# Kernel optimization log

Measured on AMD Instinct MI355X. Metric: run time of the kernel, lower is better.

## Reference

```python
import jax, jax.numpy as jnp
import numpy as np

THRESHOLD = 0.01
TOPK_RATIO = 0.7

def setup_inputs() -> dict:
    key = jax.random.key(0)
    k1, k2, k3, k4, k5 = jax.random.split(key, 5)
    B, N, F, K = 8, 2048, 512, 256
    x = jax.random.normal(k1, (B, N, F), dtype=jnp.float32)
    adj = jax.random.uniform(k2, (B, N, N), dtype=jnp.float32)
    mask = jnp.ones((B, N), dtype=jnp.float32)
    # assign_main = Linear(F->K), ReLU, Linear(K->K)
    W1 = jax.random.normal(k3, (F, K), dtype=jnp.float32) / np.sqrt(F)
    b1 = jnp.zeros((K,), dtype=jnp.float32)
    W2 = jax.random.normal(k4, (K, K), dtype=jnp.float32) / np.sqrt(K)
    b2 = jnp.zeros((K,), dtype=jnp.float32)
    return {"x": x, "adj": adj, "mask": mask, "W1": W1, "b1": b1, "W2": W2, "b2": b2}

def reference(x, adj, mask, W1, b1, W2, b2):
    B, N, Fdim = x.shape
    K = W2.shape[1]
    # soft assignment logits with masked softmax over clusters
    h = jax.nn.relu(jnp.einsum('bnf,fk->bnk', x, W1) + b1)
    logits = jnp.einsum('bnk,kl->bnl', h, W2) + b2            # [B,N,K]
    logits = logits + (-1e9) * (1.0 - mask[..., None])
    S = jax.nn.softmax(logits, axis=-1)                       # [B,N,K]
    # pooled features and pooled adjacency
    pfeat = jnp.einsum('bnk,bnf->bkf', S, x)                  # S^T x -> [B,K,F]
    mid = jnp.einsum('bnm,bmk->bnk', adj, S)                  # adj @ S
    pooled = jnp.einsum('bnk,bnl->bkl', S, mid)               # S^T adj S -> [B,K,K]
    # threshold + top-k sparsify with straight-through estimator
    topk = min(K, int(np.ceil(TOPK_RATIO * K)))
    thr_mask = (pooled >= THRESHOLD).astype(pooled.dtype)
    a_thr = pooled * thr_mask
    _, idx = jax.lax.top_k(a_thr, topk)                       # [B,K,topk]
    bi = jnp.arange(B)[:, None, None]
    ri = jnp.arange(K)[None, :, None]
    fmask = jnp.zeros_like(pooled).at[bi, ri, idx].set(1.0)
    a_sp = pooled * fmask
    a_ste = a_sp + jax.lax.stop_gradient(pooled - a_sp)       # forward == pooled
    # symmetric degree renormalization
    row_sum = a_ste.sum(axis=-1)
    d_inv_sqrt = 1.0 / jnp.sqrt(row_sum + 1e-9)
    pooled_adj = a_ste * d_inv_sqrt[:, :, None] * d_inv_sqrt[:, None, :]
    pmask = jnp.ones((B, K), dtype=x.dtype)
    return pfeat, pooled_adj, pmask
```

## Files before the change

kernel.cpp:

```cpp
#include <hip/hip_runtime.h>
#include <hip/hip_bf16.h>


typedef float f32x4 __attribute__((ext_vector_type(4)));
typedef __bf16 bf16x8 __attribute__((ext_vector_type(8)));

__device__ __forceinline__ void async_load16(const void* g, void* l) {
  __builtin_amdgcn_global_load_lds((const __attribute__((address_space(1))) void*)g,
                                   (__attribute__((address_space(3))) void*)l, 16, 0, 0);
}
__device__ __forceinline__ unsigned short f2bf(float f) {
  return __builtin_bit_cast(unsigned short, (__bf16)f);
}
__device__ __forceinline__ ushort4 f4_to_bf4(float4 v) {
  ushort4 u; u.x = f2bf(v.x); u.y = f2bf(v.y); u.z = f2bf(v.z); u.w = f2bf(v.w); return u;
}

template <int ROWS, int BK, int NT>
__device__ __forceinline__ void stage_bf16(const __bf16* __restrict__ src, long long ld,
                                           __bf16* lds, int t) {
  constexpr int GR = BK / 8;
  constexpr int N = ROWS * GR / NT;
#pragma unroll
  for (int c = 0; c < N; ++c) {
    const int idx = c * NT + t;
    const int row = idx / GR;
    const int g = idx % GR;
    const int gs = g ^ (row & (GR - 1) & 7);
    async_load16(src + (long long)row * ld + gs * 8, lds + idx * 8);
  }
}
template <int BK>
__device__ __forceinline__ bf16x8 frag(const __bf16* lds, int row, int kq) {
  constexpr int GR = BK / 8;
  const int g = kq ^ (row & (GR - 1) & 7);
  return *(const bf16x8*)(lds + row * BK + g * 8);
}

__global__ __launch_bounds__(256) void prep_weights_k(const float* __restrict__ W1,
                                                      const float* __restrict__ W2,
                                                      __bf16* __restrict__ W1T,
                                                      __bf16* __restrict__ W2T) {
  __shared__ float tile[64][65];
  int bid = blockIdx.x;
  const float* in; __bf16* out; int R, C;
  if (bid < 32) { in = W1; out = W1T; R = 512; C = 256; }
  else { bid -= 32; in = W2; out = W2T; R = 256; C = 256; }
  const int r0 = (bid >> 2) * 64, c0 = (bid & 3) * 64;
  const int tr = threadIdx.x >> 6, tc = threadIdx.x & 63;
#pragma unroll
  for (int i = 0; i < 16; ++i)
    tile[tr + i * 4][tc] = in[(long long)(r0 + tr + i * 4) * C + c0 + tc];
  __syncthreads();
#pragma unroll
  for (int i = 0; i < 16; ++i)
    out[(long long)(c0 + tr + i * 4) * R + r0 + tc] = (__bf16)tile[tc][tr + i * 4];
}

__global__ __launch_bounds__(256) void assign_fused_k(
    const float* __restrict__ x, const __bf16* __restrict__ W1T,
    const __bf16* __restrict__ W2T, const float* __restrict__ b1,
    const float* __restrict__ b2, const float* __restrict__ mask,
    __bf16* __restrict__ ST) {
  __shared__ alignas(16) __bf16 Ax[2][32 * 32];
  __shared__ alignas(16) __bf16 Bw[2][256 * 32];
  __shared__ alignas(16) __bf16 hl[32 * 264];
  __shared__ float red[2][4][32];

  const int t = threadIdx.x;
  const int lane = t & 63, wave = t >> 6;
  const int l15 = lane & 15, l4 = lane >> 4;
  const int wn = wave * 64;
  const long long row0 = (long long)blockIdx.y * 32;
  const float* Xb = x + row0 * 512;

  const int arow = t >> 3, afq = t & 7;
  const int aoff = arow * 32 + (((afq >> 1) ^ (arow & 3)) * 8) + (afq & 1) * 4;

  f32x4 acc[2][4] = {};

  float4 va = *(const float4*)(Xb + (long long)arow * 512 + afq * 4);
  stage_bf16<256, 32, 256>(W1T, 512, Bw[0], t);
  *(ushort4*)&Ax[0][aoff] = f4_to_bf4(va);
  __syncthreads();

  for (int tt = 0; tt < 16; ++tt) {
    const int cur = tt & 1, nxt = cur ^ 1;
    float4 na;
    if (tt < 15) {
      const int kk = (tt + 1) * 32;
      na = *(const float4*)(Xb + (long long)arow * 512 + kk + afq * 4);
      stage_bf16<256, 32, 256>(W1T + kk, 512, Bw[nxt], t);
    }
    bf16x8 af[2], bfr[4];
#pragma unroll
    for (int i = 0; i < 2; ++i) af[i] = frag<32>(Ax[cur], i * 16 + l15, l4);
#pragma unroll
    for (int j = 0; j < 4; ++j) bfr[j] = frag<32>(Bw[cur], wn + j * 16 + l15, l4);
#pragma unroll
    for (int i = 0; i < 2; ++i)
#pragma unroll
      for (int j = 0; j < 4; ++j)
        acc[i][j] = __builtin_amdgcn_mfma_f32_16x16x32_bf16(af[i], bfr[j], acc[i][j], 0, 0, 0);
    if (tt < 15) *(ushort4*)&Ax[nxt][aoff] = f4_to_bf4(na);
    __syncthreads();
  }

  stage_bf16<256, 32, 256>(W2T, 256, Bw[0], t);
#pragma unroll
  for (int j = 0; j < 4; ++j) {
    const int col = wn + j * 16 + l15;
    const float bv = b1[col];
#pragma unroll
    for (int i = 0; i < 2; ++i)
#pragma unroll
      for (int r = 0; r < 4; ++r)
        hl[(i * 16 + l4 * 4 + r) * 264 + col] = (__bf16)fmaxf(acc[i][j][r] + bv, 0.f);
  }
  __syncthreads();

  f32x4 acc2[2][4] = {};
  for (int tt = 0; tt < 8; ++tt) {
    const int cur = tt & 1, nxt = cur ^ 1;
    if (tt < 7) stage_bf16<256, 32, 256>(W2T + (tt + 1) * 32, 256, Bw[nxt], t);
    bf16x8 af[2], bfr[4];
#pragma unroll
    for (int i = 0; i < 2; ++i)
      af[i] = *(const bf16x8*)(&hl[(i * 16 + l15) * 264 + tt * 32 + l4 * 8]);
#pragma unroll
    for (int j = 0; j < 4; ++j) bfr[j] = frag<32>(Bw[cur], wn + j * 16 + l15, l4);
#pragma unroll
    for (int i = 0; i < 2; ++i)
#pragma unroll
      for (int j = 0; j < 4; ++j)
        acc2[i][j] = __builtin_amdgcn_mfma_f32_16x16x32_bf16(af[i], bfr[j], acc2[i][j], 0, 0, 0);
    __syncthreads();
  }

  float mb[2][4], mx[2][4], sm[2][4];
#pragma unroll
  for (int i = 0; i < 2; ++i)
#pragma unroll
    for (int r = 0; r < 4; ++r) {
      mb[i][r] = -1e9f * (1.0f - mask[row0 + i * 16 + l4 * 4 + r]);
      mx[i][r] = -3.4e38f;
      sm[i][r] = 0.f;
    }
#pragma unroll
  for (int j = 0; j < 4; ++j) {
    const float bv = b2[wn + j * 16 + l15];
#pragma unroll
    for (int i = 0; i < 2; ++i)
#pragma unroll
      for (int r = 0; r < 4; ++r) {
        const float v = acc2[i][j][r] + bv + mb[i][r];
        acc2[i][j][r] = v;
        mx[i][r] = fmaxf(mx[i][r], v);
      }
  }
#pragma unroll
  for (int i = 0; i < 2; ++i)
#pragma unroll
    for (int r = 0; r < 4; ++r) {
      float m = mx[i][r];
      m = fmaxf(m, __shfl_xor(m, 1, 64)); m = fmaxf(m, __shfl_xor(m, 2, 64));
      m = fmaxf(m, __shfl_xor(m, 4, 64)); m = fmaxf(m, __shfl_xor(m, 8, 64));
      mx[i][r] = m;
    }
  if (l15 == 0)
#pragma unroll
    for (int i = 0; i < 2; ++i)
#pragma unroll
      for (int r = 0; r < 4; ++r) red[0][wave][i * 16 + l4 * 4 + r] = mx[i][r];
  __syncthreads();
#pragma unroll
  for (int i = 0; i < 2; ++i)
#pragma unroll
    for (int r = 0; r < 4; ++r) {
      const int rl = i * 16 + l4 * 4 + r;
      mx[i][r] = fmaxf(fmaxf(red[0][0][rl], red[0][1][rl]),
                       fmaxf(red[0][2][rl], red[0][3][rl]));
    }
#pragma unroll
  for (int j = 0; j < 4; ++j)
#pragma unroll
    for (int i = 0; i < 2; ++i)
#pragma unroll
      for (int r = 0; r < 4; ++r) {
        const float e = __expf(acc2[i][j][r] - mx[i][r]);
        acc2[i][j][r] = e;
        sm[i][r] += e;
      }
#pragma unroll
  for (int i = 0; i < 2; ++i)
#pragma unroll
    for (int r = 0; r < 4; ++r) {
      float s = sm[i][r];
      s += __shfl_xor(s, 1, 64); s += __shfl_xor(s, 2, 64);
      s += __shfl_xor(s, 4, 64); s += __shfl_xor(s, 8, 64);
      sm[i][r] = s;
    }
  if (l15 == 0)
#pragma unroll
    for (int i = 0; i < 2; ++i)
#pragma unroll
      for (int r = 0; r < 4; ++r) red[1][wave][i * 16 + l4 * 4 + r] = sm[i][r];
  __syncthreads();
  float inv[2][4];
#pragma unroll
  for (int i = 0; i < 2; ++i)
#pragma unroll
    for (int r = 0; r < 4; ++r) {
      const int rl = i * 16 + l4 * 4 + r;
      inv[i][r] = 1.0f / (red[1][0][rl] + red[1][1][rl] + red[1][2][rl] + red[1][3][rl]);
    }
  const long long bb = row0 >> 11;
  const long long n0 = row0 & 2047;
  __bf16* Sb = ST + bb * 524288;
#pragma unroll
  for (int j = 0; j < 4; ++j) {
    const int col = wn + j * 16 + l15;
#pragma unroll
    for (int i = 0; i < 2; ++i) {
      ushort4 u;
      u.x = f2bf(acc2[i][j][0] * inv[i][0]);
      u.y = f2bf(acc2[i][j][1] * inv[i][1]);
      u.z = f2bf(acc2[i][j][2] * inv[i][2]);
      u.w = f2bf(acc2[i][j][3] * inv[i][3]);
      *(ushort4*)(Sb + (long long)col * 2048 + n0 + i * 16 + l4 * 4) = u;
    }
  }
}

__global__ __launch_bounds__(256) void gemm_adj_k(const float* __restrict__ adj,
                                                  const __bf16* __restrict__ ST,
                                                  __bf16* __restrict__ midT) {
  __shared__ alignas(16) __bf16 Aa[2][32 * 64];
  __shared__ alignas(16) __bf16 Bs[2][256 * 64];
  const int t = threadIdx.x;
  const int lane = t & 63, wave = t >> 6;
  const int l15 = lane & 15, l4 = lane >> 4;
  const int wn = wave * 64;
  const int bz = blockIdx.z;
  const long long r0 = (long long)blockIdx.y * 32;
  const float* Ab = adj + (long long)bz * 4194304 + r0 * 2048;
  const __bf16* Bb = ST + (long long)bz * 524288;

  const int arow = t >> 4, afq = t & 15;
  const int arow1 = arow + 16;
  const int aoff0 = arow * 64 + (((afq >> 1) ^ (arow & 7)) * 8) + (afq & 1) * 4;
  const int aoff1 = arow1 * 64 + (((afq >> 1) ^ (arow1 & 7)) * 8) + (afq & 1) * 4;

  f32x4 acc[2][4] = {};

  float4 va0 = *(const float4*)(Ab + (long long)arow * 2048 + afq * 4);
  float4 va1 = *(const float4*)(Ab + (long long)arow1 * 2048 + afq * 4);
  stage_bf16<256, 64, 256>(Bb, 2048, Bs[0], t);
  *(ushort4*)&Aa[0][aoff0] = f4_to_bf4(va0);
  *(ushort4*)&Aa[0][aoff1] = f4_to_bf4(va1);
  __syncthreads();

  for (int tt = 0; tt < 32; ++tt) {
    const int cur = tt & 1, nxt = cur ^ 1;
    float4 na0, na1;
    if (tt < 31) {
      const int kk = (tt + 1) * 64;
      na0 = *(const float4*)(Ab + (long long)arow * 2048 + kk + afq * 4);
      na1 = *(const float4*)(Ab + (long long)arow1 * 2048 + kk + afq * 4);
      stage_bf16<256, 64, 256>(Bb + kk, 2048, Bs[nxt], t);
    }
#pragma unroll
    for (int ks = 0; ks < 2; ++ks) {
      bf16x8 af[2], bfr[4];
#pragma unroll
      for (int i = 0; i < 2; ++i) af[i] = frag<64>(Aa[cur], i * 16 + l15, ks * 4 + l4);
#pragma unroll
      for (int j = 0; j < 4; ++j) bfr[j] = frag<64>(Bs[cur], wn + j * 16 + l15, ks * 4 + l4);
#pragma unroll
      for (int i = 0; i < 2; ++i)
#pragma unroll
        for (int j = 0; j < 4; ++j)
          acc[i][j] = __builtin_amdgcn_mfma_f32_16x16x32_bf16(af[i], bfr[j], acc[i][j], 0, 0, 0);
    }
    if (tt < 31) {
      *(ushort4*)&Aa[nxt][aoff0] = f4_to_bf4(na0);
      *(ushort4*)&Aa[nxt][aoff1] = f4_to_bf4(na1);
    }
    __syncthreads();
  }

  __bf16* Cb = midT + (long long)bz * 524288;
#pragma unroll
  for (int j = 0; j < 4; ++j) {
    const int l = wn + j * 16 + l15;
#pragma unroll
    for (int i = 0; i < 2; ++i) {
      ushort4 u;
      u.x = f2bf(acc[i][j][0]); u.y = f2bf(acc[i][j][1]);
      u.z = f2bf(acc[i][j][2]); u.w = f2bf(acc[i][j][3]);
      *(ushort4*)(Cb + (long long)l * 2048 + r0 + i * 16 + l4 * 4) = u;
    }
  }
}

__global__ __launch_bounds__(256) void gemm_pool_k(const __bf16* __restrict__ ST,
                                                   const __bf16* __restrict__ midT,
                                                   float* __restrict__ partP) {
  __shared__ alignas(16) __bf16 As[2][64 * 64];
  __shared__ alignas(16) __bf16 Bs[2][64 * 64];
  const int t = threadIdx.x;
  const int lane = t & 63, wave = t >> 6;
  const int l15 = lane & 15, l4 = lane >> 4;
  const int wm = (wave >> 1) * 32, wn = (wave & 1) * 32;
  const int b = blockIdx.z >> 2, ks = blockIdx.z & 3;
  const long long row0 = (long long)blockIdx.y * 64, col0 = (long long)blockIdx.x * 64;
  const __bf16* Ab = ST + (long long)b * 524288 + row0 * 2048 + ks * 512;
  const __bf16* Bb = midT + (long long)b * 524288 + col0 * 2048 + ks * 512;

  f32x4 acc[2][2] = {};
  stage_bf16<64, 64, 256>(Ab, 2048, As[0], t);
  stage_bf16<64, 64, 256>(Bb, 2048, Bs[0], t);
  __syncthreads();
  for (int tt = 0; tt < 8; ++tt) {
    const int cur = tt & 1, nxt = cur ^ 1;
    if (tt < 7) {
      stage_bf16<64, 64, 256>(Ab + (tt + 1) * 64, 2048, As[nxt], t);
      stage_bf16<64, 64, 256>(Bb + (tt + 1) * 64, 2048, Bs[nxt], t);
    }
#pragma unroll
    for (int ksb = 0; ksb < 2; ++ksb) {
      bf16x8 af[2], bfr[2];
#pragma unroll
      for (int i = 0; i < 2; ++i) af[i] = frag<64>(As[cur], wm + i * 16 + l15, ksb * 4 + l4);
#pragma unroll
      for (int j = 0; j < 2; ++j) bfr[j] = frag<64>(Bs[cur], wn + j * 16 + l15, ksb * 4 + l4);
#pragma unroll
      for (int i = 0; i < 2; ++i)
#pragma unroll
        for (int j = 0; j < 2; ++j)
          acc[i][j] = __builtin_amdgcn_mfma_f32_16x16x32_bf16(af[i], bfr[j], acc[i][j], 0, 0, 0);
    }
    __syncthreads();
  }
  float* out = partP + (long long)blockIdx.z * 65536;
#pragma unroll
  for (int i = 0; i < 2; ++i)
#pragma unroll
    for (int j = 0; j < 2; ++j)
#pragma unroll
      for (int r = 0; r < 4; ++r)
        out[(row0 + wm + i * 16 + l4 * 4 + r) * 256 + col0 + wn + j * 16 + l15] = acc[i][j][r];
}

__global__ __launch_bounds__(512) void gemm_feat_k(const __bf16* __restrict__ ST,
                                                   const float* __restrict__ x,
                                                   float* __restrict__ partF) {
  __shared__ alignas(16) __bf16 As[2][256 * 32];
  __shared__ alignas(16) __bf16 Bx[2][128 * 40];
  const int t = threadIdx.x;
  const int lane = t & 63, wave = t >> 6;
  const int l15 = lane & 15, l4 = lane >> 4;
  const int wm = (wave >> 2) * 128, wn = (wave & 3) * 32;
  const int b = blockIdx.z >> 3, ks = blockIdx.z & 7;
  const int f0 = blockIdx.x * 128;
  const __bf16* Ab = ST + (long long)b * 524288 + ks * 256;
  const float* Xb = x + (long long)b * 1048576 + (long long)ks * 256 * 512 + f0;

  const int xn0 = t >> 5, xfq = t & 31;
  f32x4 acc[8][2] = {};

  auto ldx = [&](int kk, int c) -> float4 {
    return *(const float4*)(Xb + (long long)(kk + c * 16 + xn0) * 512 + xfq * 4);
  };
  auto stx = [&](int buf, float4 v, int c) {
    const int n = c * 16 + xn0;
    Bx[buf][(xfq * 4 + 0) * 40 + n] = (__bf16)v.x;
    Bx[buf][(xfq * 4 + 1) * 40 + n] = (__bf16)v.y;
    Bx[buf][(xfq * 4 + 2) * 40 + n] = (__bf16)v.z;
    Bx[buf][(xfq * 4 + 3) * 40 + n] = (__bf16)v.w;
  };

  float4 vb0 = ldx(0, 0), vb1 = ldx(0, 1);
  stage_bf16<256, 32, 512>(Ab, 2048, As[0], t);
  stx(0, vb0, 0); stx(0, vb1, 1);
  __syncthreads();
  for (int tt = 0; tt < 8; ++tt) {
    const int cur = tt & 1, nxt = cur ^ 1;
    float4 n0, n1;
    if (tt < 7) {
      n0 = ldx((tt + 1) * 32, 0); n1 = ldx((tt + 1) * 32, 1);
      stage_bf16<256, 32, 512>(Ab + (tt + 1) * 32, 2048, As[nxt], t);
    }
    bf16x8 af[8], bfr[2];
#pragma unroll
    for (int i = 0; i < 8; ++i) af[i] = frag<32>(As[cur], wm + i * 16 + l15, l4);
#pragma unroll
    for (int j = 0; j < 2; ++j)
      bfr[j] = *(const bf16x8*)(&Bx[cur][(wn + j * 16 + l15) * 40 + l4 * 8]);
#pragma unroll
    for (int i = 0; i < 8; ++i)
#pragma unroll
      for (int j = 0; j < 2; ++j)
        acc[i][j] = __builtin_amdgcn_mfma_f32_16x16x32_bf16(af[i], bfr[j], acc[i][j], 0, 0, 0);
    if (tt < 7) { stx(nxt, n0, 0); stx(nxt, n1, 1); }
    __syncthreads();
  }
  float* out = partF + (long long)blockIdx.z * 131072;
#pragma unroll
  for (int i = 0; i < 8; ++i)
#pragma unroll
    for (int j = 0; j < 2; ++j)
#pragma unroll
      for (int r = 0; r < 4; ++r)
        out[(wm + i * 16 + l4 * 4 + r) * 512 + f0 + wn + j * 16 + l15] = acc[i][j][r];
}

__global__ __launch_bounds__(256) void reduce_pool_k(const float* __restrict__ partP,
                                                     float* __restrict__ pooled,
                                                     float* __restrict__ dinv) {
  const int gr = blockIdx.x * 4 + (threadIdx.x >> 6);
  const int lane = threadIdx.x & 63;
  const int b = gr >> 8, row = gr & 255;
  const long long base = (long long)b * 4 * 65536 + (long long)row * 256;
  float s = 0.f;
#pragma unroll
  for (int q = 0; q < 4; ++q) {
    const int c = lane + q * 64;
    float v = partP[base + c] + partP[base + 65536 + c] +
              partP[base + 131072 + c] + partP[base + 196608 + c];
    pooled[(long long)gr * 256 + c] = v;
    s += v;
  }
#pragma unroll
  for (int o = 32; o > 0; o >>= 1) s += __shfl_xor(s, o, 64);
  if (lane == 0) dinv[gr] = rsqrtf(s + 1e-9f);
}

__global__ __launch_bounds__(256) void reduce_feat_k(const float* __restrict__ partF,
                                                     float* __restrict__ pfeat) {
  const long long p = blockIdx.x * 256LL + threadIdx.x;
  const int b = (int)(p >> 15), rc = (int)(p & 32767);
  const float4* src = (const float4*)partF;
  float4 a = {0.f, 0.f, 0.f, 0.f};
#pragma unroll
  for (int ks = 0; ks < 8; ++ks) {
    const float4 v = src[(long long)(b * 8 + ks) * 32768 + rc];
    a.x += v.x; a.y += v.y; a.z += v.z; a.w += v.w;
  }
  ((float4*)pfeat)[p] = a;
}

__global__ __launch_bounds__(256) void finalize_k(const float* __restrict__ pooled,
                                                  const float* __restrict__ dinv,
                                                  float* __restrict__ outAdj,
                                                  float* __restrict__ pmask) {
  const long long i = blockIdx.x * 256LL + threadIdx.x;
  const int c = (int)(i & 255);
  const int r = (int)((i >> 8) & 255);
  const int b = (int)(i >> 16);
  outAdj[i] = pooled[i] * dinv[b * 256 + r] * dinv[b * 256 + c];
  if (i < 2048) pmask[i] = 1.0f;
}

extern "C" void kernel_launch(void* const* d_in, const int* in_sizes, int n_in,
                              void* d_out, int out_size, void* d_ws, size_t ws_size,
                              hipStream_t stream) {
  (void)in_sizes; (void)n_in; (void)out_size; (void)ws_size;
  const float* x    = (const float*)d_in[0];
  const float* adj  = (const float*)d_in[1];
  const float* mask = (const float*)d_in[2];
  const float* W1   = (const float*)d_in[3];
  const float* b1   = (const float*)d_in[4];
  const float* W2   = (const float*)d_in[5];
  const float* b2   = (const float*)d_in[6];

  char* ws = (char*)d_ws;
  __bf16* ST     = (__bf16*)(ws + 0);
  __bf16* midT   = (__bf16*)(ws + 8388608);
  float*  partP  = (float*)(ws + 16777216);
  float*  partF  = (float*)(ws + 25165824);
  float*  pooled = (float*)(ws + 58720256);
  float*  dinv   = (float*)(ws + 60817408);
  __bf16* W1T    = (__bf16*)(ws + 60825600);
  __bf16* W2T    = (__bf16*)(ws + 61087744);

  float* pfeat  = (float*)d_out;
  float* outAdj = (float*)d_out + 1048576;
  float* pmask  = (float*)d_out + 1572864;

  prep_weights_k<<<48, 256, 0, stream>>>(W1, W2, W1T, W2T);
  assign_fused_k<<<dim3(1, 512, 1), 256, 0, stream>>>(x, W1T, W2T, b1, b2, mask, ST);
  gemm_feat_k<<<dim3(4, 1, 64), 512, 0, stream>>>(ST, x, partF);
  reduce_feat_k<<<1024, 256, 0, stream>>>(partF, pfeat);
  gemm_adj_k<<<dim3(1, 64, 8), 256, 0, stream>>>(adj, ST, midT);
  gemm_pool_k<<<dim3(4, 4, 32), 256, 0, stream>>>(ST, midT, partP);
  reduce_pool_k<<<512, 256, 0, stream>>>(partP, pooled, dinv);
  finalize_k<<<2048, 256, 0, stream>>>(pooled, dinv, outAdj, pmask);
}
```

Measured before the change: 133.5 us.

## Hand-pipeline GEMM kernels with explicit waitcnt, sched barriers and larger adj tiles

```diff
diff --git a/kernel.cpp b/kernel.cpp
--- a/kernel.cpp
+++ b/kernel.cpp
@@ -4,6 +4,17 @@
 
 typedef float f32x4 __attribute__((ext_vector_type(4)));
 typedef __bf16 bf16x8 __attribute__((ext_vector_type(8)));
+
+#define VMCNT(n) asm volatile("s_waitcnt vmcnt(" #n ")" ::: "memory")
+#define LGKM0    asm volatile("s_waitcnt lgkmcnt(0)" ::: "memory")
+#define SCHEDB   __builtin_amdgcn_sched_barrier(0)
+#define BARRIER                                        \
+  do {                                                 \
+    LGKM0;                                             \
+    __builtin_amdgcn_s_barrier();                      \
+    asm volatile("" ::: "memory");                     \
+    SCHEDB;                                            \
+  } while (0)
 
 __device__ __forceinline__ void async_load16(const void* g, void* l) {
   __builtin_amdgcn_global_load_lds((const __attribute__((address_space(1))) void*)g,
@@ -57,6 +68,23 @@
     out[(long long)(c0 + tr + i * 4) * R + r0 + tc] = (__bf16)tile[tc][tr + i * 4];
 }
 
+__device__ __forceinline__ void asg_compute(const __bf16* __restrict__ Abuf,
+                                            const __bf16* __restrict__ Bbuf,
+                                            f32x4 (&acc)[2][4], int wn, int l15, int l4) {
+  bf16x8 af[2], bf[4];
+#pragma unroll
+  for (int i = 0; i < 2; ++i) af[i] = frag<32>(Abuf, i * 16 + l15, l4);
+#pragma unroll
+  for (int j = 0; j < 4; ++j) bf[j] = frag<32>(Bbuf, wn + j * 16 + l15, l4);
+  __builtin_amdgcn_s_setprio(1);
+#pragma unroll
+  for (int i = 0; i < 2; ++i)
+#pragma unroll
+    for (int j = 0; j < 4; ++j)
+      acc[i][j] = __builtin_amdgcn_mfma_f32_16x16x32_bf16(af[i], bf[j], acc[i][j], 0, 0, 0);
+  __builtin_amdgcn_s_setprio(0);
+}
+
 __global__ __launch_bounds__(256) void assign_fused_k(
     const float* __restrict__ x, const __bf16* __restrict__ W1T,
     const __bf16* __restrict__ W2T, const float* __restrict__ b1,
@@ -71,42 +99,63 @@
   const int lane = t & 63, wave = t >> 6;
   const int l15 = lane & 15, l4 = lane >> 4;
   const int wn = wave * 64;
-  const long long row0 = (long long)blockIdx.y * 32;
+  const long long row0 = (long long)blockIdx.x * 32;
   const float* Xb = x + row0 * 512;
 
   const int arow = t >> 3, afq = t & 7;
-  const int aoff = arow * 32 + (((afq >> 1) ^ (arow & 3)) * 8) + (afq & 1) * 4;
+  const int ag = afq >> 1;
+  const int aoff = arow * 32 + ((ag ^ (arow & 3)) * 8) + (afq & 1) * 4;
+
+  auto ldx = [&](int tile) -> float4 {
+    return *(const float4*)(Xb + (long long)arow * 512 + tile * 32 + afq * 4);
+  };
+  auto sta = [&](__bf16* dst, float4 v) { *(ushort4*)&dst[aoff] = f4_to_bf4(v); };
 
   f32x4 acc[2][4] = {};
 
-  float4 va = *(const float4*)(Xb + (long long)arow * 512 + afq * 4);
+  float4 xA = ldx(0);
+  SCHEDB;
   stage_bf16<256, 32, 256>(W1T, 512, Bw[0], t);
-  *(ushort4*)&Ax[0][aoff] = f4_to_bf4(va);
-  __syncthreads();
-
-  for (int tt = 0; tt < 16; ++tt) {
-    const int cur = tt & 1, nxt = cur ^ 1;
-    float4 na;
-    if (tt < 15) {
-      const int kk = (tt + 1) * 32;
-      na = *(const float4*)(Xb + (long long)arow * 512 + kk + afq * 4);
-      stage_bf16<256, 32, 256>(W1T + kk, 512, Bw[nxt], t);
-    }
-    bf16x8 af[2], bfr[4];
-#pragma unroll
-    for (int i = 0; i < 2; ++i) af[i] = frag<32>(Ax[cur], i * 16 + l15, l4);
-#pragma unroll
-    for (int j = 0; j < 4; ++j) bfr[j] = frag<32>(Bw[cur], wn + j * 16 + l15, l4);
-#pragma unroll
-    for (int i = 0; i < 2; ++i)
-#pragma unroll
-      for (int j = 0; j < 4; ++j)
-        acc[i][j] = __builtin_amdgcn_mfma_f32_16x16x32_bf16(af[i], bfr[j], acc[i][j], 0, 0, 0);
-    if (tt < 15) *(ushort4*)&Ax[nxt][aoff] = f4_to_bf4(na);
-    __syncthreads();
-  }
+  SCHEDB;
+  VMCNT(4); SCHEDB;
+  sta(Ax[0], xA);
+  float4 xB = ldx(1);
+  SCHEDB;
+  VMCNT(1); SCHEDB;
+  BARRIER;
+
+#pragma unroll 1
+  for (int tt = 0; tt < 14; tt += 2) {
+    stage_bf16<256, 32, 256>(W1T + (tt + 1) * 32, 512, Bw[1], t);
+    SCHEDB;
+    xA = ldx(tt + 2);
+    SCHEDB;
+    asg_compute(Ax[0], Bw[0], acc, wn, l15, l4);
+    VMCNT(5); SCHEDB;
+    sta(Ax[1], xB);
+    VMCNT(1); SCHEDB;
+    BARRIER;
+    stage_bf16<256, 32, 256>(W1T + (tt + 2) * 32, 512, Bw[0], t);
+    SCHEDB;
+    xB = ldx(tt + 3);
+    SCHEDB;
+    asg_compute(Ax[1], Bw[1], acc, wn, l15, l4);
+    VMCNT(5); SCHEDB;
+    sta(Ax[0], xA);
+    VMCNT(1); SCHEDB;
+    BARRIER;
+  }
+  stage_bf16<256, 32, 256>(W1T + 15 * 32, 512, Bw[1], t);
+  SCHEDB;
+  asg_compute(Ax[0], Bw[0], acc, wn, l15, l4);
+  VMCNT(4); SCHEDB;
+  sta(Ax[1], xB);
+  VMCNT(0); SCHEDB;
+  BARRIER;
+  asg_compute(Ax[1], Bw[1], acc, wn, l15, l4);
 
   stage_bf16<256, 32, 256>(W2T, 256, Bw[0], t);
+  SCHEDB;
 #pragma unroll
   for (int j = 0; j < 4; ++j) {
     const int col = wn + j * 16 + l15;
@@ -117,24 +166,28 @@
       for (int r = 0; r < 4; ++r)
         hl[(i * 16 + l4 * 4 + r) * 264 + col] = (__bf16)fmaxf(acc[i][j][r] + bv, 0.f);
   }
-  __syncthreads();
+  VMCNT(0); SCHEDB;
+  BARRIER;
 
   f32x4 acc2[2][4] = {};
+#pragma unroll 1
   for (int tt = 0; tt < 8; ++tt) {
-    const int cur = tt & 1, nxt = cur ^ 1;
-    if (tt < 7) stage_bf16<256, 32, 256>(W2T + (tt + 1) * 32, 256, Bw[nxt], t);
-    bf16x8 af[2], bfr[4];
+    if (tt < 7) stage_bf16<256, 32, 256>(W2T + (tt + 1) * 32, 256, Bw[(tt & 1) ^ 1], t);
+    SCHEDB;
+    const __bf16* Bc = Bw[tt & 1];
+    bf16x8 af[2], bf[4];
 #pragma unroll
     for (int i = 0; i < 2; ++i)
       af[i] = *(const bf16x8*)(&hl[(i * 16 + l15) * 264 + tt * 32 + l4 * 8]);
 #pragma unroll
-    for (int j = 0; j < 4; ++j) bfr[j] = frag<32>(Bw[cur], wn + j * 16 + l15, l4);
+    for (int j = 0; j < 4; ++j) bf[j] = frag<32>(Bc, wn + j * 16 + l15, l4);
 #pragma unroll
     for (int i = 0; i < 2; ++i)
 #pragma unroll
       for (int j = 0; j < 4; ++j)
-        acc2[i][j] = __builtin_amdgcn_mfma_f32_16x16x32_bf16(af[i], bfr[j], acc2[i][j], 0, 0, 0);
-    __syncthreads();
+        acc2[i][j] = __builtin_amdgcn_mfma_f32_16x16x32_bf16(af[i], bf[j], acc2[i][j], 0, 0, 0);
+    VMCNT(0); SCHEDB;
+    BARRIER;
   }
 
   float mb[2][4], mx[2][4], sm[2][4];
@@ -232,62 +285,97 @@
   }
 }
 
-__global__ __launch_bounds__(256) void gemm_adj_k(const float* __restrict__ adj,
+__device__ __forceinline__ void adj_compute(const __bf16* __restrict__ Abuf,
+                                            const __bf16* __restrict__ Bbuf,
+                                            f32x4 (&acc)[2][4],
+                                            int wm, int wn, int l15, int l4) {
+#pragma unroll
+  for (int ks = 0; ks < 2; ++ks) {
+    bf16x8 af[2], bf[4];
+#pragma unroll
+    for (int i = 0; i < 2; ++i) af[i] = frag<64>(Abuf, wm + i * 16 + l15, ks * 4 + l4);
+#pragma unroll
+    for (int j = 0; j < 4; ++j) bf[j] = frag<64>(Bbuf, wn + j * 16 + l15, ks * 4 + l4);
+    __builtin_amdgcn_s_setprio(1);
+#pragma unroll
+    for (int i = 0; i < 2; ++i)
+#pragma unroll
+      for (int j = 0; j < 4; ++j)
+        acc[i][j] = __builtin_amdgcn_mfma_f32_16x16x32_bf16(af[i], bf[j], acc[i][j], 0, 0, 0);
+    __builtin_amdgcn_s_setprio(0);
+  }
+}
+
+__global__ __launch_bounds__(512) void gemm_adj_k(const float* __restrict__ adj,
                                                   const __bf16* __restrict__ ST,
                                                   __bf16* __restrict__ midT) {
-  __shared__ alignas(16) __bf16 Aa[2][32 * 64];
+  __shared__ alignas(16) __bf16 Aa[2][64 * 64];
   __shared__ alignas(16) __bf16 Bs[2][256 * 64];
   const int t = threadIdx.x;
   const int lane = t & 63, wave = t >> 6;
   const int l15 = lane & 15, l4 = lane >> 4;
-  const int wn = wave * 64;
-  const int bz = blockIdx.z;
-  const long long r0 = (long long)blockIdx.y * 32;
+  const int wm = (wave >> 2) * 32, wn = (wave & 3) * 64;
+  const int id = blockIdx.x;
+  const int bz = id & 7;
+  const long long r0 = (long long)(id >> 3) * 64;
   const float* Ab = adj + (long long)bz * 4194304 + r0 * 2048;
   const __bf16* Bb = ST + (long long)bz * 524288;
 
   const int arow = t >> 4, afq = t & 15;
-  const int arow1 = arow + 16;
-  const int aoff0 = arow * 64 + (((afq >> 1) ^ (arow & 7)) * 8) + (afq & 1) * 4;
-  const int aoff1 = arow1 * 64 + (((afq >> 1) ^ (arow1 & 7)) * 8) + (afq & 1) * 4;
+  const int ag = afq >> 1;
+  const int aoff0 = arow * 64 + ((ag ^ (arow & 7)) * 8) + (afq & 1) * 4;
+  const int aoff1 = (arow + 32) * 64 + ((ag ^ ((arow + 32) & 7)) * 8) + (afq & 1) * 4;
+
+  auto lda4 = [&](int tile, int half) -> float4 {
+    return *(const float4*)(Ab + (long long)(arow + half * 32) * 2048 + tile * 64 + afq * 4);
+  };
+  auto sta = [&](__bf16* dst, float4 v0, float4 v1) {
+    *(ushort4*)&dst[aoff0] = f4_to_bf4(v0);
+    *(ushort4*)&dst[aoff1] = f4_to_bf4(v1);
+  };
 
   f32x4 acc[2][4] = {};
 
-  float4 va0 = *(const float4*)(Ab + (long long)arow * 2048 + afq * 4);
-  float4 va1 = *(const float4*)(Ab + (long long)arow1 * 2048 + afq * 4);
-  stage_bf16<256, 64, 256>(Bb, 2048, Bs[0], t);
-  *(ushort4*)&Aa[0][aoff0] = f4_to_bf4(va0);
-  *(ushort4*)&Aa[0][aoff1] = f4_to_bf4(va1);
-  __syncthreads();
-
-  for (int tt = 0; tt < 32; ++tt) {
-    const int cur = tt & 1, nxt = cur ^ 1;
-    float4 na0, na1;
-    if (tt < 31) {
-      const int kk = (tt + 1) * 64;
-      na0 = *(const float4*)(Ab + (long long)arow * 2048 + kk + afq * 4);
-      na1 = *(const float4*)(Ab + (long long)arow1 * 2048 + kk + afq * 4);
-      stage_bf16<256, 64, 256>(Bb + kk, 2048, Bs[nxt], t);
-    }
-#pragma unroll
-    for (int ks = 0; ks < 2; ++ks) {
-      bf16x8 af[2], bfr[4];
-#pragma unroll
-      for (int i = 0; i < 2; ++i) af[i] = frag<64>(Aa[cur], i * 16 + l15, ks * 4 + l4);
-#pragma unroll
-      for (int j = 0; j < 4; ++j) bfr[j] = frag<64>(Bs[cur], wn + j * 16 + l15, ks * 4 + l4);
-#pragma unroll
-      for (int i = 0; i < 2; ++i)
-#pragma unroll
-        for (int j = 0; j < 4; ++j)
-          acc[i][j] = __builtin_amdgcn_mfma_f32_16x16x32_bf16(af[i], bfr[j], acc[i][j], 0, 0, 0);
-    }
-    if (tt < 31) {
-      *(ushort4*)&Aa[nxt][aoff0] = f4_to_bf4(na0);
-      *(ushort4*)&Aa[nxt][aoff1] = f4_to_bf4(na1);
-    }
-    __syncthreads();
-  }
+  float4 aA0 = lda4(0, 0), aA1 = lda4(0, 1);
+  SCHEDB;
+  stage_bf16<256, 64, 512>(Bb, 2048, Bs[0], t);
+  SCHEDB;
+  VMCNT(4); SCHEDB;
+  sta(Aa[0], aA0, aA1);
+  float4 aB0 = lda4(1, 0), aB1 = lda4(1, 1);
+  SCHEDB;
+  VMCNT(2); SCHEDB;
+  BARRIER;
+
+#pragma unroll 1
+  for (int tt = 0; tt < 30; tt += 2) {
+    stage_bf16<256, 64, 512>(Bb + (tt + 1) * 64, 2048, Bs[1], t);
+    SCHEDB;
+    aA0 = lda4(tt + 2, 0); aA1 = lda4(tt + 2, 1);
+    SCHEDB;
+    adj_compute(Aa[0], Bs[0], acc, wm, wn, l15, l4);
+    VMCNT(6); SCHEDB;
+    sta(Aa[1], aB0, aB1);
+    VMCNT(2); SCHEDB;
+    BARRIER;
+    stage_bf16<256, 64, 512>(Bb + (tt + 2) * 64, 2048, Bs[0], t);
+    SCHEDB;
+    aB0 = lda4(tt + 3, 0); aB1 = lda4(tt + 3, 1);
+    SCHEDB;
+    adj_compute(Aa[1], Bs[1], acc, wm, wn, l15, l4);
+    VMCNT(6); SCHEDB;
+    sta(Aa[0], aA0, aA1);
+    VMCNT(2); SCHEDB;
+    BARRIER;
+  }
+  stage_bf16<256, 64, 512>(Bb + 31 * 64, 2048, Bs[1], t);
+  SCHEDB;
+  adj_compute(Aa[0], Bs[0], acc, wm, wn, l15, l4);
+  VMCNT(4); SCHEDB;
+  sta(Aa[1], aB0, aB1);
+  VMCNT(0); SCHEDB;
+  BARRIER;
+  adj_compute(Aa[1], Bs[1], acc, wm, wn, l15, l4);
 
   __bf16* Cb = midT + (long long)bz * 524288;
 #pragma unroll
@@ -298,9 +386,108 @@
       ushort4 u;
       u.x = f2bf(acc[i][j][0]); u.y = f2bf(acc[i][j][1]);
       u.z = f2bf(acc[i][j][2]); u.w = f2bf(acc[i][j][3]);
-      *(ushort4*)(Cb + (long long)l * 2048 + r0 + i * 16 + l4 * 4) = u;
-    }
-  }
+      *(ushort4*)(Cb + (long long)l * 2048 + r0 + wm + i * 16 + l4 * 4) = u;
+    }
+  }
+}
+
+__device__ __forceinline__ void feat_compute(const __bf16* __restrict__ Abuf,
+                                             const __bf16* __restrict__ Bbuf,
+                                             f32x4 (&acc)[8][2],
+                                             int wm, int wn, int l15, int l4) {
+  bf16x8 af[8], bf[2];
+#pragma unroll
+  for (int i = 0; i < 8; ++i) af[i] = frag<32>(Abuf, wm + i * 16 + l15, l4);
+#pragma unroll
+  for (int j = 0; j < 2; ++j)
+    bf[j] = *(const bf16x8*)(&Bbuf[(wn + j * 16 + l15) * 40 + l4 * 8]);
+  __builtin_amdgcn_s_setprio(1);
+#pragma unroll
+  for (int i = 0; i < 8; ++i)
+#pragma unroll
+    for (int j = 0; j < 2; ++j)
+      acc[i][j] = __builtin_amdgcn_mfma_f32_16x16x32_bf16(af[i], bf[j], acc[i][j], 0, 0, 0);
+  __builtin_amdgcn_s_setprio(0);
+}
+
+__global__ __launch_bounds__(512) void gemm_feat_k(const __bf16* __restrict__ ST,
+                                                   const float* __restrict__ x,
+                                                   float* __restrict__ partF) {
+  __shared__ alignas(16) __bf16 As[2][256 * 32];
+  __shared__ alignas(16) __bf16 Bx[2][128 * 40];
+  const int t = threadIdx.x;
+  const int lane = t & 63, wave = t >> 6;
+  const int l15 = lane & 15, l4 = lane >> 4;
+  const int wm = (wave >> 2) * 128, wn = (wave & 3) * 32;
+  const int gid = blockIdx.x;
+  const int b = gid & 7, ks = gid >> 5, fblk = (gid >> 3) & 3;
+  const int f0 = fblk * 128;
+  const __bf16* Ab = ST + (long long)b * 524288 + ks * 256;
+  const float* Xb = x + (long long)b * 1048576 + (long long)ks * 256 * 512 + f0;
+
+  const int xn0 = t >> 5, xfq = t & 31;
+  f32x4 acc[8][2] = {};
+
+  auto ldx = [&](int tile, int half) -> float4 {
+    return *(const float4*)(Xb + (long long)(tile * 32 + half * 16 + xn0) * 512 + xfq * 4);
+  };
+  auto stx = [&](__bf16* dst, float4 v, int half) {
+    const int n = half * 16 + xn0;
+    dst[(xfq * 4 + 0) * 40 + n] = (__bf16)v.x;
+    dst[(xfq * 4 + 1) * 40 + n] = (__bf16)v.y;
+    dst[(xfq * 4 + 2) * 40 + n] = (__bf16)v.z;
+    dst[(xfq * 4 + 3) * 40 + n] = (__bf16)v.w;
+  };
+
+  float4 xA0 = ldx(0, 0), xA1 = ldx(0, 1);
+  SCHEDB;
+  stage_bf16<256, 32, 512>(Ab, 2048, As[0], t);
+  SCHEDB;
+  VMCNT(2); SCHEDB;
+  stx(Bx[0], xA0, 0); stx(Bx[0], xA1, 1);
+  float4 xB0 = ldx(1, 0), xB1 = ldx(1, 1);
+  SCHEDB;
+  VMCNT(2); SCHEDB;
+  BARRIER;
+
+#pragma unroll 1
+  for (int tt = 0; tt < 6; tt += 2) {
+    stage_bf16<256, 32, 512>(Ab + (tt + 1) * 32, 2048, As[1], t);
+    SCHEDB;
+    xA0 = ldx(tt + 2, 0); xA1 = ldx(tt + 2, 1);
+    SCHEDB;
+    feat_compute(As[0], Bx[0], acc, wm, wn, l15, l4);
+    VMCNT(4); SCHEDB;
+    stx(Bx[1], xB0, 0); stx(Bx[1], xB1, 1);
+    VMCNT(2); SCHEDB;
+    BARRIER;
+    stage_bf16<256, 32, 512>(Ab + (tt + 2) * 32, 2048, As[0], t);
+    SCHEDB;
+    xB0 = ldx(tt + 3, 0); xB1 = ldx(tt + 3, 1);
+    SCHEDB;
+    feat_compute(As[1], Bx[1], acc, wm, wn, l15, l4);
+    VMCNT(4); SCHEDB;
+    stx(Bx[0], xA0, 0); stx(Bx[0], xA1, 1);
+    VMCNT(2); SCHEDB;
+    BARRIER;
+  }
+  stage_bf16<256, 32, 512>(Ab + 7 * 32, 2048, As[1], t);
+  SCHEDB;
+  feat_compute(As[0], Bx[0], acc, wm, wn, l15, l4);
+  VMCNT(2); SCHEDB;
+  stx(Bx[1], xB0, 0); stx(Bx[1], xB1, 1);
+  VMCNT(0); SCHEDB;
+  BARRIER;
+  feat_compute(As[1], Bx[1], acc, wm, wn, l15, l4);
+
+  float* out = partF + ((long long)b * 8 + ks) * 131072;
+#pragma unroll
+  for (int i = 0; i < 8; ++i)
+#pragma unroll
+    for (int j = 0; j < 2; ++j)
+#pragma unroll
+      for (int r = 0; r < 4; ++r)
+        out[(wm + i * 16 + l4 * 4 + r) * 512 + f0 + wn + j * 16 + l15] = acc[i][j][r];
 }
 
 __global__ __launch_bounds__(256) void gemm_pool_k(const __bf16* __restrict__ ST,
@@ -352,69 +539,6 @@
         out[(row0 + wm + i * 16 + l4 * 4 + r) * 256 + col0 + wn + j * 16 + l15] = acc[i][j][r];
 }
 
-__global__ __launch_bounds__(512) void gemm_feat_k(const __bf16* __restrict__ ST,
-                                                   const float* __restrict__ x,
-                                                   float* __restrict__ partF) {
-  __shared__ alignas(16) __bf16 As[2][256 * 32];
-  __shared__ alignas(16) __bf16 Bx[2][128 * 40];
-  const int t = threadIdx.x;
-  const int lane = t & 63, wave = t >> 6;
-  const int l15 = lane & 15, l4 = lane >> 4;
-  const int wm = (wave >> 2) * 128, wn = (wave & 3) * 32;
-  const int b = blockIdx.z >> 3, ks = blockIdx.z & 7;
-  const int f0 = blockIdx.x * 128;
-  const __bf16* Ab = ST + (long long)b * 524288 + ks * 256;
-  const float* Xb = x + (long long)b * 1048576 + (long long)ks * 256 * 512 + f0;
-
-  const int xn0 = t >> 5, xfq = t & 31;
-  f32x4 acc[8][2] = {};
-
-  auto ldx = [&](int kk, int c) -> float4 {
-    return *(const float4*)(Xb + (long long)(kk + c * 16 + xn0) * 512 + xfq * 4);
-  };
-  auto stx = [&](int buf, float4 v, int c) {
-    const int n = c * 16 + xn0;
-    Bx[buf][(xfq * 4 + 0) * 40 + n] = (__bf16)v.x;
-    Bx[buf][(xfq * 4 + 1) * 40 + n] = (__bf16)v.y;
-    Bx[buf][(xfq * 4 + 2) * 40 + n] = (__bf16)v.z;
-    Bx[buf][(xfq * 4 + 3) * 40 + n] = (__bf16)v.w;
-  };
-
-  float4 vb0 = ldx(0, 0), vb1 = ldx(0, 1);
-  stage_bf16<256, 32, 512>(Ab, 2048, As[0], t);
-  stx(0, vb0, 0); stx(0, vb1, 1);
-  __syncthreads();
-  for (int tt = 0; tt < 8; ++tt) {
-    const int cur = tt & 1, nxt = cur ^ 1;
-    float4 n0, n1;
-    if (tt < 7) {
-      n0 = ldx((tt + 1) * 32, 0); n1 = ldx((tt + 1) * 32, 1);
-      stage_bf16<256, 32, 512>(Ab + (tt + 1) * 32, 2048, As[nxt], t);
-    }
-    bf16x8 af[8], bfr[2];
-#pragma unroll
-    for (int i = 0; i < 8; ++i) af[i] = frag<32>(As[cur], wm + i * 16 + l15, l4);
-#pragma unroll
-    for (int j = 0; j < 2; ++j)
-      bfr[j] = *(const bf16x8*)(&Bx[cur][(wn + j * 16 + l15) * 40 + l4 * 8]);
-#pragma unroll
-    for (int i = 0; i < 8; ++i)
-#pragma unroll
-      for (int j = 0; j < 2; ++j)
-        acc[i][j] = __builtin_amdgcn_mfma_f32_16x16x32_bf16(af[i], bfr[j], acc[i][j], 0, 0, 0);
-    if (tt < 7) { stx(nxt, n0, 0); stx(nxt, n1, 1); }
-    __syncthreads();
-  }
-  float* out = partF + (long long)blockIdx.z * 131072;
-#pragma unroll
-  for (int i = 0; i < 8; ++i)
-#pragma unroll
-    for (int j = 0; j < 2; ++j)
-#pragma unroll
-      for (int r = 0; r < 4; ++r)
-        out[(wm + i * 16 + l4 * 4 + r) * 512 + f0 + wn + j * 16 + l15] = acc[i][j][r];
-}
-
 __global__ __launch_bounds__(256) void reduce_pool_k(const float* __restrict__ partP,
                                                      float* __restrict__ pooled,
                                                      float* __restrict__ dinv) {
@@ -489,10 +613,10 @@
   float* pmask  = (float*)d_out + 1572864;
 
   prep_weights_k<<<48, 256, 0, stream>>>(W1, W2, W1T, W2T);
-  assign_fused_k<<<dim3(1, 512, 1), 256, 0, stream>>>(x, W1T, W2T, b1, b2, mask, ST);
-  gemm_feat_k<<<dim3(4, 1, 64), 512, 0, stream>>>(ST, x, partF);
+  assign_fused_k<<<512, 256, 0, stream>>>(x, W1T, W2T, b1, b2, mask, ST);
+  gemm_feat_k<<<256, 512, 0, stream>>>(ST, x, partF);
   reduce_feat_k<<<1024, 256, 0, stream>>>(partF, pfeat);
-  gemm_adj_k<<<dim3(1, 64, 8), 256, 0, stream>>>(adj, ST, midT);
+  gemm_adj_k<<<256, 512, 0, stream>>>(adj, ST, midT);
   gemm_pool_k<<<dim3(4, 4, 32), 256, 0, stream>>>(ST, midT, partP);
   reduce_pool_k<<<512, 256, 0, stream>>>(partP, pooled, dinv);
   finalize_k<<<2048, 256, 0, stream>>>(pooled, dinv, outAdj, pmask);
```

New measurement: 116.5 us. -12.7%, faster.
